# Kernel tuning notes

Hardware: AMD Instinct MI355X
Metric: run time of the kernel (lower is better)

## Reference

```python
import jax, jax.numpy as jnp
import numpy as np

NUM_LAYERS = 2
HIDDEN = 512


def _lstm_layer(x_tbh, h0, c0, Wih, Whh, bih, bhh):
    """Run one LSTM layer over time.
    x_tbh: [T,B,I]; h0,c0: [B,H]; Wih: [4H,I]; Whh: [4H,H]; bih,bhh: [4H].
    Gate order follows torch.nn.LSTMCell: i, f, g, o.
    Returns (outputs [T,B,H], (h_T, c_T)).
    """
    bias = bih + bhh

    def step(carry, x_t):
        h, c = carry
        gates = x_t @ Wih.T + h @ Whh.T + bias  # [B,4H]
        i, f, g, o = jnp.split(gates, 4, axis=-1)
        i = jax.nn.sigmoid(i)
        f = jax.nn.sigmoid(f)
        g = jnp.tanh(g)
        o = jax.nn.sigmoid(o)
        c_new = f * c + i * g
        h_new = o * jnp.tanh(c_new)
        return (h_new, c_new), h_new

    (h_T, c_T), outs = jax.lax.scan(step, (h0, c0), x_tbh)
    return outs, (h_T, c_T)


def setup_inputs() -> dict:
    key = jax.random.key(0)
    ks = jax.random.split(key, 7)
    B, T, I, H, L = 32, 1024, 512, HIDDEN, NUM_LAYERS
    scale = 1.0 / np.sqrt(H)
    return {
        "input": jax.random.normal(ks[0], (B, T, I), dtype=jnp.float32),
        "h0": jax.random.normal(ks[1], (L, B, H), dtype=jnp.float32),
        "c0": jax.random.normal(ks[2], (L, B, H), dtype=jnp.float32),
        "W_ih": jax.random.normal(ks[3], (L, 4 * H, I), dtype=jnp.float32) * scale,
        "W_hh": jax.random.normal(ks[4], (L, 4 * H, H), dtype=jnp.float32) * scale,
        "b_ih": jax.random.normal(ks[5], (L, 4 * H), dtype=jnp.float32) * scale,
        "b_hh": jax.random.normal(ks[6], (L, 4 * H), dtype=jnp.float32) * scale,
    }


def reference(input, h0, c0, W_ih, W_hh, b_ih, b_hh):
    # batch_first=True -> transpose to time-major for the scan
    x = jnp.transpose(input, (1, 0, 2))  # [T,B,I]
    h_outs, c_outs = [], []
    for l in range(NUM_LAYERS):
        x, (h_T, c_T) = _lstm_layer(x, h0[l], c0[l], W_ih[l], W_hh[l], b_ih[l], b_hh[l])
        h_outs.append(h_T)
        c_outs.append(c_T)
    out = jnp.transpose(x, (1, 0, 2))  # back to [B,T,H]
    return out, (jnp.stack(h_outs), jnp.stack(c_outs))
```

## Files before the change

### kernel.cpp

```cpp
#include <hip/hip_runtime.h>
#include <math.h>

#define T_STEPS 1024
#define BATCH   32
#define HID     512
#define G4      2048
#define KDIM    1024
#define NWG     128
#define WGL     64
#define JPW     8
#define APAD    1032
#define FPAD    32

#define OUT_ELEMS   (BATCH * T_STEPS * HID)
#define H_OFF       OUT_ELEMS
#define C_OFF       (OUT_ELEMS + 2 * BATCH * HID)

typedef __attribute__((ext_vector_type(8)))  short short8;
typedef __attribute__((ext_vector_type(16))) float f32x16;

__device__ __forceinline__ unsigned short f2bf(float f) {
    union { float f; unsigned u; } v; v.f = f;
    unsigned r = v.u + 0x7fffu + ((v.u >> 16) & 1u);
    return (unsigned short)(r >> 16);
}

__device__ __forceinline__ float sigm(float x)  { return 1.0f / (1.0f + __expf(-x)); }
__device__ __forceinline__ float ftanh(float x) { return 1.0f - 2.0f / (__expf(2.0f * x) + 1.0f); }

__device__ __forceinline__ short8 load_b128_llc(const void* p) {
    short8 r;
    asm volatile("global_load_dwordx4 %0, %1, off sc0 sc1"
                 : "=v"(r) : "v"(p));
    return r;
}

__device__ __forceinline__ void g_arrive(unsigned* flags, int wg, unsigned epoch, int tid) {
    asm volatile("s_waitcnt vmcnt(0)" ::: "memory");
    __syncthreads();
    if (tid == 0)
        __hip_atomic_store(&flags[wg * FPAD], epoch, __ATOMIC_RELAXED, __HIP_MEMORY_SCOPE_AGENT);
}

__device__ __forceinline__ void g_wait(unsigned* flags, unsigned epoch, int tid) {
    if (tid < NWG) {
        while (__hip_atomic_load(&flags[tid * FPAD], __ATOMIC_RELAXED, __HIP_MEMORY_SCOPE_AGENT) < epoch)
            __builtin_amdgcn_s_sleep(1);
    }
    __syncthreads();
}

__global__ void init_flags(unsigned* flags) {
    for (int i = threadIdx.x; i < NWG * FPAD; i += 256) flags[i] = 0u;
}

__global__ void __launch_bounds__(256, 1)
lstm_persist(const float* __restrict__ x_in,
             const float* __restrict__ h0,
             const float* __restrict__ c0,
             const float* __restrict__ Wih,
             const float* __restrict__ Whh,
             const float* __restrict__ bih,
             const float* __restrict__ bhh,
             float* __restrict__ out,
             unsigned* __restrict__ flags,
             unsigned short* __restrict__ h1ring,
             unsigned short* __restrict__ h2ring,
             unsigned short* __restrict__ xbf,
             int use_xbf)
{
    __shared__ __attribute__((aligned(16))) short Wbuf[32 * APAD];
    __shared__ float gatebuf[4][BATCH][36];
    __shared__ float biasbuf[32];

    const int wg    = blockIdx.x;
    const int layer = (wg >= WGL) ? 1 : 0;
    const int wgl   = wg - layer * WGL;
    const int jbase = wgl * JPW;
    const int tid   = threadIdx.x;

    if (use_xbf) {
        const size_t total4 = (size_t)BATCH * T_STEPS * HID / 4;
        unsigned long long* dst = (unsigned long long*)xbf;
        for (size_t idx = (size_t)wg * 256 + tid; idx < total4; idx += (size_t)NWG * 256) {
            float4 v = *(const float4*)(x_in + idx * 4);
            unsigned long long pk = (unsigned long long)f2bf(v.x)
                                  | ((unsigned long long)f2bf(v.y) << 16)
                                  | ((unsigned long long)f2bf(v.z) << 32)
                                  | ((unsigned long long)f2bf(v.w) << 48);
            dst[idx] = pk;
        }
        __builtin_amdgcn_fence(__ATOMIC_RELEASE, "agent");
    }

    {
        const int lr = tid >> 3;
        const int g0 = tid & 7;
        const int gg = lr >> 3, jloc = lr & 7;
        const int r  = gg * HID + jbase + jloc;
        const float* srcA = Wih + ((size_t)layer * G4 + r) * HID;
        const float* srcB = Whh + ((size_t)layer * G4 + r) * HID;
        short* dstrow = &Wbuf[lr * APAD];
        #pragma unroll
        for (int i = 0; i < 16; ++i) {
            int g = g0 + 8 * i;
            const float* src = (g < 64) ? (srcA + g * 8) : (srcB + (g - 64) * 8);
            float4 v0 = *(const float4*)(src);
            float4 v1 = *(const float4*)(src + 4);
            short8 p;
            p[0] = (short)f2bf(v0.x); p[1] = (short)f2bf(v0.y);
            p[2] = (short)f2bf(v0.z); p[3] = (short)f2bf(v0.w);
            p[4] = (short)f2bf(v1.x); p[5] = (short)f2bf(v1.y);
            p[6] = (short)f2bf(v1.z); p[7] = (short)f2bf(v1.w);
            *(short8*)(dstrow + g * 8) = p;
        }
    }
    if (tid < 32) {
        const int g = tid >> 3, jloc = tid & 7;
        const int r = g * HID + jbase + jloc;
        biasbuf[tid] = bih[(size_t)layer * G4 + r] + bhh[(size_t)layer * G4 + r];
    }

    const int m  = tid >> 3;
    const int jl = tid & 7;
    const int jg = jbase + jl;

    float creg = c0[((size_t)layer * BATCH + m) * HID + jg];

    {
        unsigned hb = (unsigned)f2bf(h0[((size_t)layer * BATCH + m) * HID + jg]);
        unsigned ob = __shfl_xor(hb, 1);
        if ((tid & 1) == 0) {
            unsigned val = hb | (ob << 16);
            unsigned short* ring = (layer == 0) ? h1ring : h2ring;
            if (layer == 0) {
                unsigned* p = (unsigned*)(ring + ((size_t)1 * BATCH + m) * HID + (jg & ~1));
                __hip_atomic_store(p, val, __ATOMIC_RELAXED, __HIP_MEMORY_SCOPE_AGENT);
            } else {
                unsigned* p0 = (unsigned*)(ring + ((size_t)0 * BATCH + m) * HID + (jg & ~1));
                unsigned* p1 = (unsigned*)(ring + ((size_t)1 * BATCH + m) * HID + (jg & ~1));
                __hip_atomic_store(p0, val, __ATOMIC_RELAXED, __HIP_MEMORY_SCOPE_AGENT);
                __hip_atomic_store(p1, val, __ATOMIC_RELAXED, __HIP_MEMORY_SCOPE_AGENT);
            }
        }
    }

    g_arrive(flags, wg, 1u, tid);
    g_wait(flags, 1u, tid);
    __builtin_amdgcn_fence(__ATOMIC_ACQUIRE, "agent");

    const int lane = tid & 63;
    const int wv   = tid >> 6;
    const int hi   = lane >> 5;
    const int arow = lane & 31;
    const int kq   = (wv & 1) * 256;
    const bool xw  = (wv < 2);

    const short* wrow = &Wbuf[arow * APAD + wv * 256 + hi * 8];

    short8 afr[16];

#define PREFETCH_X(tt)                                                        \
    do {                                                                      \
        if (use_xbf) {                                                        \
            const short* bx = (const short*)xbf +                             \
                ((size_t)arow * T_STEPS + (tt)) * HID + kq + hi * 8;          \
            _Pragma("unroll")                                                 \
            for (int j = 0; j < 16; ++j)                                      \
                afr[j] = *(const short8*)(bx + j * 16);                       \
        } else {                                                              \
            const float* fx = x_in +                                          \
                ((size_t)arow * T_STEPS + (tt)) * HID + kq + hi * 8;          \
            _Pragma("unroll")                                                 \
            for (int j = 0; j < 16; ++j) {                                    \
                float4 v0 = *(const float4*)(fx + j * 16);                    \
                float4 v1 = *(const float4*)(fx + j * 16 + 4);                \
                short8 p;                                                     \
                p[0] = (short)f2bf(v0.x); p[1] = (short)f2bf(v0.y);           \
                p[2] = (short)f2bf(v0.z); p[3] = (short)f2bf(v0.w);           \
                p[4] = (short)f2bf(v1.x); p[5] = (short)f2bf(v1.y);           \
                p[6] = (short)f2bf(v1.z); p[7] = (short)f2bf(v1.w);           \
                afr[j] = p;                                                   \
            }                                                                 \
        }                                                                     \
    } while (0)

    if (layer == 0 && xw) PREFETCH_X(0);

    for (int s = 0; s <= T_STEPS; ++s) {
        const int t = (layer == 0) ? s : s - 1;
        const bool active = (t >= 0) && (t < T_STEPS);
        float hv = 0.0f;
        if (active) {
            const int rs = (s + 1) & 1;

            if (!(layer == 0 && xw)) {
                const unsigned short* ring =
                    (layer == 0) ? h1ring : (xw ? h1ring : h2ring);
                const short* base = (const short*)ring +
                    ((size_t)rs * BATCH + arow) * HID + kq + hi * 8;
                #pragma unroll
                for (int j = 0; j < 16; ++j)
                    afr[j] = load_b128_llc(base + j * 16);
                asm volatile("s_waitcnt vmcnt(0)" ::: "memory");
                __builtin_amdgcn_sched_barrier(0);
            }

            f32x16 acc0, acc1;
            #pragma unroll
            for (int r = 0; r < 16; ++r) { acc0[r] = 0.0f; acc1[r] = 0.0f; }
            #pragma unroll
            for (int j = 0; j < 16; j += 2) {
                short8 b0 = *(const short8*)(wrow + j * 16);
                short8 b1 = *(const short8*)(wrow + j * 16 + 16);
                acc0 = __builtin_amdgcn_mfma_f32_32x32x16_bf16(afr[j],     b0, acc0, 0, 0, 0);
                acc1 = __builtin_amdgcn_mfma_f32_32x32x16_bf16(afr[j + 1], b1, acc1, 0, 0, 0);
            }
            #pragma unroll
            for (int r = 0; r < 16; ++r)
                gatebuf[wv][(r & 3) + 8 * (r >> 2) + 4 * hi][arow] = acc0[r] + acc1[r];
            __syncthreads();

            float gi = gatebuf[0][m][jl]      + gatebuf[1][m][jl]
                     + gatebuf[2][m][jl]      + gatebuf[3][m][jl]      + biasbuf[jl];
            float gf = gatebuf[0][m][8 + jl]  + gatebuf[1][m][8 + jl]
                     + gatebuf[2][m][8 + jl]  + gatebuf[3][m][8 + jl]  + biasbuf[8 + jl];
            float gg = gatebuf[0][m][16 + jl] + gatebuf[1][m][16 + jl]
                     + gatebuf[2][m][16 + jl] + gatebuf[3][m][16 + jl] + biasbuf[16 + jl];
            float go = gatebuf[0][m][24 + jl] + gatebuf[1][m][24 + jl]
                     + gatebuf[2][m][24 + jl] + gatebuf[3][m][24 + jl] + biasbuf[24 + jl];
            float iv = sigm(gi), fv = sigm(gf), gv = ftanh(gg), ov = sigm(go);
            creg = fv * creg + iv * gv;
            hv = ov * ftanh(creg);

            {
                const int wslot = s & 1;
                unsigned hb = (unsigned)f2bf(hv);
                unsigned ob = __shfl_xor(hb, 1);
                if ((tid & 1) == 0) {
                    unsigned val = hb | (ob << 16);
                    unsigned short* ringw = (layer == 0) ? h1ring : h2ring;
                    unsigned* p = (unsigned*)(ringw + ((size_t)wslot * BATCH + m) * HID + (jg & ~1));
                    __hip_atomic_store(p, val, __ATOMIC_RELAXED, __HIP_MEMORY_SCOPE_AGENT);
                }
            }
            if (t == T_STEPS - 1)
                out[H_OFF + ((size_t)layer * BATCH + m) * HID + jg] = hv;
        }

        const bool last = (s == T_STEPS);
        if (!last) g_arrive(flags, wg, (unsigned)(s + 2), tid);

        if (active && layer == 1)
            out[((size_t)m * T_STEPS + t) * HID + jg] = hv;
        if (layer == 0 && xw && active && t + 1 < T_STEPS)
            PREFETCH_X(t + 1);

        if (!last) g_wait(flags, (unsigned)(s + 2), tid);
    }

    out[C_OFF + ((size_t)layer * BATCH + m) * HID + jg] = creg;
#undef PREFETCH_X
}

extern "C" void kernel_launch(void* const* d_in, const int* in_sizes, int n_in,
                              void* d_out, int out_size, void* d_ws, size_t ws_size,
                              hipStream_t stream) {
    const float* x   = (const float*)d_in[0];
    const float* h0  = (const float*)d_in[1];
    const float* c0  = (const float*)d_in[2];
    const float* Wih = (const float*)d_in[3];
    const float* Whh = (const float*)d_in[4];
    const float* bih = (const float*)d_in[5];
    const float* bhh = (const float*)d_in[6];
    float* out = (float*)d_out;

    unsigned char* ws = (unsigned char*)d_ws;
    unsigned* flags = (unsigned*)ws;
    unsigned short* h1ring = (unsigned short*)(ws + 16384);
    unsigned short* h2ring = h1ring + 2 * BATCH * HID;
    unsigned short* xbf    = h2ring + 2 * BATCH * HID;

    const size_t xbf_need = 16384 + 2 * 64 * 1024 +
                            (size_t)BATCH * T_STEPS * HID * 2 + 4096;
    int use_xbf = (ws_size >= xbf_need) ? 1 : 0;

    hipLaunchKernelGGL(init_flags, dim3(1), dim3(256), 0, stream, flags);

    void* args[] = { (void*)&x, (void*)&h0, (void*)&c0, (void*)&Wih, (void*)&Whh,
                     (void*)&bih, (void*)&bhh, (void*)&out, (void*)&flags,
                     (void*)&h1ring, (void*)&h2ring, (void*)&xbf, (void*)&use_xbf };
    hipError_t e = hipLaunchCooperativeKernel((void*)lstm_persist, dim3(NWG), dim3(256),
                                              args, 0, stream);
    if (e != hipSuccess) {
        hipLaunchKernelGGL(lstm_persist, dim3(NWG), dim3(256), 0, stream,
                           x, h0, c0, Wih, Whh, bih, bhh, out, flags,
                           h1ring, h2ring, xbf, use_xbf);
    }
}
```

Baseline: 4.652 ms.

## Replace global barrier with per-layer flag waits, 8-slot h1 ring, register-resident weights

Replaces the full all-workgroup barrier each step with targeted flag polling. Layer 1 waits only on layer 0's flags for its input h1 and on its own layer's flags for h2. Layer 0 waits on its own peers, with a lagged check on layer 1 so the 8-slot h1 ring is not overwritten early. Layer 1 now runs two steps behind and prefetches the h1 input fragments before the barrier completes. Weights move from LDS into per-lane bf16 MFMA operand registers, which removes LDS reads from the inner loop at the cost of higher register pressure and more complex correctness invariants.

```diff
diff --git a/kernel.cpp b/kernel.cpp
--- a/kernel.cpp
+++ b/kernel.cpp
@@ -5,16 +5,20 @@
 #define BATCH   32
 #define HID     512
 #define G4      2048
-#define KDIM    1024
 #define NWG     128
 #define WGL     64
 #define JPW     8
-#define APAD    1032
 #define FPAD    32
-
-#define OUT_ELEMS   (BATCH * T_STEPS * HID)
-#define H_OFF       OUT_ELEMS
-#define C_OFF       (OUT_ELEMS + 2 * BATCH * HID)
+#define RD      8
+
+#define WS_FLAGS 0
+#define WS_H1    16384
+#define WS_H2    278528
+#define WS_XBF   344064
+
+#define OUT_ELEMS (BATCH * T_STEPS * HID)
+#define H_OFF OUT_ELEMS
+#define C_OFF (OUT_ELEMS + 2 * BATCH * HID)
 
 typedef __attribute__((ext_vector_type(8)))  short short8;
 typedef __attribute__((ext_vector_type(16))) float f32x16;
@@ -24,14 +28,12 @@
     unsigned r = v.u + 0x7fffu + ((v.u >> 16) & 1u);
     return (unsigned short)(r >> 16);
 }
-
 __device__ __forceinline__ float sigm(float x)  { return 1.0f / (1.0f + __expf(-x)); }
 __device__ __forceinline__ float ftanh(float x) { return 1.0f - 2.0f / (__expf(2.0f * x) + 1.0f); }
 
-__device__ __forceinline__ short8 load_b128_llc(const void* p) {
+__device__ __forceinline__ short8 ld_llc(const void* p) {
     short8 r;
-    asm volatile("global_load_dwordx4 %0, %1, off sc0 sc1"
-                 : "=v"(r) : "v"(p));
+    asm volatile("global_load_dwordx4 %0, %1, off sc0 sc1" : "=v"(r) : "v"(p));
     return r;
 }
 
@@ -42,12 +44,9 @@
         __hip_atomic_store(&flags[wg * FPAD], epoch, __ATOMIC_RELAXED, __HIP_MEMORY_SCOPE_AGENT);
 }
 
-__device__ __forceinline__ void g_wait(unsigned* flags, unsigned epoch, int tid) {
-    if (tid < NWG) {
-        while (__hip_atomic_load(&flags[tid * FPAD], __ATOMIC_RELAXED, __HIP_MEMORY_SCOPE_AGENT) < epoch)
-            __builtin_amdgcn_s_sleep(1);
-    }
-    __syncthreads();
+__device__ __forceinline__ void poll_ge(const unsigned* p, unsigned epoch) {
+    while (__hip_atomic_load(p, __ATOMIC_RELAXED, __HIP_MEMORY_SCOPE_AGENT) < epoch)
+        __builtin_amdgcn_s_sleep(1);
 }
 
 __global__ void init_flags(unsigned* flags) {
@@ -63,13 +62,9 @@
              const float* __restrict__ bih,
              const float* __restrict__ bhh,
              float* __restrict__ out,
-             unsigned* __restrict__ flags,
-             unsigned short* __restrict__ h1ring,
-             unsigned short* __restrict__ h2ring,
-             unsigned short* __restrict__ xbf,
+             unsigned char* __restrict__ ws,
              int use_xbf)
 {
-    __shared__ __attribute__((aligned(16))) short Wbuf[32 * APAD];
     __shared__ float gatebuf[4][BATCH][36];
     __shared__ float biasbuf[32];
 
@@ -78,6 +73,11 @@
     const int wgl   = wg - layer * WGL;
     const int jbase = wgl * JPW;
     const int tid   = threadIdx.x;
+
+    unsigned* flags = (unsigned*)(ws + WS_FLAGS);
+    unsigned short* h1ring = (unsigned short*)(ws + WS_H1);
+    unsigned short* h2ring = (unsigned short*)(ws + WS_H2);
+    unsigned short* xbf    = (unsigned short*)(ws + WS_XBF);
 
     if (use_xbf) {
         const size_t total4 = (size_t)BATCH * T_STEPS * HID / 4;
@@ -93,32 +93,32 @@
         __builtin_amdgcn_fence(__ATOMIC_RELEASE, "agent");
     }
 
-    {
-        const int lr = tid >> 3;
-        const int g0 = tid & 7;
-        const int gg = lr >> 3, jloc = lr & 7;
-        const int r  = gg * HID + jbase + jloc;
-        const float* srcA = Wih + ((size_t)layer * G4 + r) * HID;
-        const float* srcB = Whh + ((size_t)layer * G4 + r) * HID;
-        short* dstrow = &Wbuf[lr * APAD];
-        #pragma unroll
-        for (int i = 0; i < 16; ++i) {
-            int g = g0 + 8 * i;
-            const float* src = (g < 64) ? (srcA + g * 8) : (srcB + (g - 64) * 8);
-            float4 v0 = *(const float4*)(src);
-            float4 v1 = *(const float4*)(src + 4);
-            short8 p;
-            p[0] = (short)f2bf(v0.x); p[1] = (short)f2bf(v0.y);
-            p[2] = (short)f2bf(v0.z); p[3] = (short)f2bf(v0.w);
-            p[4] = (short)f2bf(v1.x); p[5] = (short)f2bf(v1.y);
-            p[6] = (short)f2bf(v1.z); p[7] = (short)f2bf(v1.w);
-            *(short8*)(dstrow + g * 8) = p;
-        }
-    }
     if (tid < 32) {
         const int g = tid >> 3, jloc = tid & 7;
         const int r = g * HID + jbase + jloc;
         biasbuf[tid] = bih[(size_t)layer * G4 + r] + bhh[(size_t)layer * G4 + r];
+    }
+
+    const int lane = tid & 63;
+    const int wv   = tid >> 6;
+    const int hi   = lane >> 5;
+    const int l31  = lane & 31;
+    const int kb   = (wv & 1) * 256;
+
+    short8 bW[16];
+    {
+        const float* Wsel = ((wv < 2) ? Wih : Whh) + (size_t)layer * G4 * HID;
+        const int r = (l31 >> 3) * HID + jbase + (l31 & 7);
+        const float* wr = Wsel + (size_t)r * HID + kb + hi * 8;
+        #pragma unroll
+        for (int j = 0; j < 16; ++j) {
+            float4 v0 = *(const float4*)(wr + j * 16);
+            float4 v1 = *(const float4*)(wr + j * 16 + 4);
+            short8 p;
+            p[0]=(short)f2bf(v0.x); p[1]=(short)f2bf(v0.y); p[2]=(short)f2bf(v0.z); p[3]=(short)f2bf(v0.w);
+            p[4]=(short)f2bf(v1.x); p[5]=(short)f2bf(v1.y); p[6]=(short)f2bf(v1.z); p[7]=(short)f2bf(v1.w);
+            bW[j] = p;
+        }
     }
 
     const int m  = tid >> 3;
@@ -132,13 +132,12 @@
         unsigned ob = __shfl_xor(hb, 1);
         if ((tid & 1) == 0) {
             unsigned val = hb | (ob << 16);
-            unsigned short* ring = (layer == 0) ? h1ring : h2ring;
             if (layer == 0) {
-                unsigned* p = (unsigned*)(ring + ((size_t)1 * BATCH + m) * HID + (jg & ~1));
+                unsigned* p = (unsigned*)(h1ring + ((size_t)7 * BATCH + m) * HID + (jg & ~1));
                 __hip_atomic_store(p, val, __ATOMIC_RELAXED, __HIP_MEMORY_SCOPE_AGENT);
             } else {
-                unsigned* p0 = (unsigned*)(ring + ((size_t)0 * BATCH + m) * HID + (jg & ~1));
-                unsigned* p1 = (unsigned*)(ring + ((size_t)1 * BATCH + m) * HID + (jg & ~1));
+                unsigned* p0 = (unsigned*)(h2ring + ((size_t)0 * BATCH + m) * HID + (jg & ~1));
+                unsigned* p1 = (unsigned*)(h2ring + ((size_t)1 * BATCH + m) * HID + (jg & ~1));
                 __hip_atomic_store(p0, val, __ATOMIC_RELAXED, __HIP_MEMORY_SCOPE_AGENT);
                 __hip_atomic_store(p1, val, __ATOMIC_RELAXED, __HIP_MEMORY_SCOPE_AGENT);
             }
@@ -146,85 +145,79 @@
     }
 
     g_arrive(flags, wg, 1u, tid);
-    g_wait(flags, 1u, tid);
+    if (tid < NWG) poll_ge(flags + tid * FPAD, 1u);
+    __syncthreads();
     __builtin_amdgcn_fence(__ATOMIC_ACQUIRE, "agent");
 
-    const int lane = tid & 63;
-    const int wv   = tid >> 6;
-    const int hi   = lane >> 5;
-    const int arow = lane & 31;
-    const int kq   = (wv & 1) * 256;
-    const bool xw  = (wv < 2);
-
-    const short* wrow = &Wbuf[arow * APAD + wv * 256 + hi * 8];
+    const unsigned* fL0 = flags;
+    const unsigned* fL1 = flags + WGL * FPAD;
 
     short8 afr[16];
 
-#define PREFETCH_X(tt)                                                        \
+#define PREFX(tt)                                                             \
     do {                                                                      \
         if (use_xbf) {                                                        \
             const short* bx = (const short*)xbf +                             \
-                ((size_t)arow * T_STEPS + (tt)) * HID + kq + hi * 8;          \
+                ((size_t)l31 * T_STEPS + (tt)) * HID + kb + hi * 8;           \
             _Pragma("unroll")                                                 \
             for (int j = 0; j < 16; ++j)                                      \
                 afr[j] = *(const short8*)(bx + j * 16);                       \
         } else {                                                              \
             const float* fx = x_in +                                          \
-                ((size_t)arow * T_STEPS + (tt)) * HID + kq + hi * 8;          \
+                ((size_t)l31 * T_STEPS + (tt)) * HID + kb + hi * 8;           \
             _Pragma("unroll")                                                 \
             for (int j = 0; j < 16; ++j) {                                    \
                 float4 v0 = *(const float4*)(fx + j * 16);                    \
                 float4 v1 = *(const float4*)(fx + j * 16 + 4);                \
                 short8 p;                                                     \
-                p[0] = (short)f2bf(v0.x); p[1] = (short)f2bf(v0.y);           \
-                p[2] = (short)f2bf(v0.z); p[3] = (short)f2bf(v0.w);           \
-                p[4] = (short)f2bf(v1.x); p[5] = (short)f2bf(v1.y);           \
-                p[6] = (short)f2bf(v1.z); p[7] = (short)f2bf(v1.w);           \
+                p[0]=(short)f2bf(v0.x); p[1]=(short)f2bf(v0.y);               \
+                p[2]=(short)f2bf(v0.z); p[3]=(short)f2bf(v0.w);               \
+                p[4]=(short)f2bf(v1.x); p[5]=(short)f2bf(v1.y);               \
+                p[6]=(short)f2bf(v1.z); p[7]=(short)f2bf(v1.w);               \
                 afr[j] = p;                                                   \
             }                                                                 \
         }                                                                     \
     } while (0)
 
-    if (layer == 0 && xw) PREFETCH_X(0);
-
-    for (int s = 0; s <= T_STEPS; ++s) {
-        const int t = (layer == 0) ? s : s - 1;
+    if (layer == 0 && wv < 2) PREFX(0);
+
+    const int SE = T_STEPS + 2;
+    for (int s = 0; s <= SE; ++s) {
+        const int t = (layer == 0) ? s : s - 2;
         const bool active = (t >= 0) && (t < T_STEPS);
+        const bool last = (s == SE);
         float hv = 0.0f;
+
         if (active) {
-            const int rs = (s + 1) & 1;
-
-            if (!(layer == 0 && xw)) {
-                const unsigned short* ring =
-                    (layer == 0) ? h1ring : (xw ? h1ring : h2ring);
+            if (wv >= 2) {
+                const unsigned short* ring = (layer == 0) ? h1ring : h2ring;
+                const size_t slot = (layer == 0) ? (size_t)((s - 1) & 7)
+                                                 : (size_t)((s + 1) & 1);
                 const short* base = (const short*)ring +
-                    ((size_t)rs * BATCH + arow) * HID + kq + hi * 8;
+                    (slot * BATCH + l31) * HID + kb + hi * 8;
                 #pragma unroll
-                for (int j = 0; j < 16; ++j)
-                    afr[j] = load_b128_llc(base + j * 16);
-                asm volatile("s_waitcnt vmcnt(0)" ::: "memory");
-                __builtin_amdgcn_sched_barrier(0);
-            }
+                for (int j = 0; j < 16; ++j) afr[j] = ld_llc(base + j * 16);
+            }
+            asm volatile("s_waitcnt vmcnt(0)" ::: "memory");
+            __builtin_amdgcn_sched_barrier(0);
 
             f32x16 acc0, acc1;
             #pragma unroll
-            for (int r = 0; r < 16; ++r) { acc0[r] = 0.0f; acc1[r] = 0.0f; }
+            for (int r = 0; r < 16; ++r) { acc0[r] = 0.f; acc1[r] = 0.f; }
             #pragma unroll
             for (int j = 0; j < 16; j += 2) {
-                short8 b0 = *(const short8*)(wrow + j * 16);
-                short8 b1 = *(const short8*)(wrow + j * 16 + 16);
-                acc0 = __builtin_amdgcn_mfma_f32_32x32x16_bf16(afr[j],     b0, acc0, 0, 0, 0);
-                acc1 = __builtin_amdgcn_mfma_f32_32x32x16_bf16(afr[j + 1], b1, acc1, 0, 0, 0);
+                acc0 = __builtin_amdgcn_mfma_f32_32x32x16_bf16(afr[j],     bW[j],     acc0, 0, 0, 0);
+                acc1 = __builtin_amdgcn_mfma_f32_32x32x16_bf16(afr[j + 1], bW[j + 1], acc1, 0, 0, 0);
             }
             #pragma unroll
             for (int r = 0; r < 16; ++r)
-                gatebuf[wv][(r & 3) + 8 * (r >> 2) + 4 * hi][arow] = acc0[r] + acc1[r];
+                gatebuf[wv][(r & 3) + 8 * (r >> 2) + 4 * hi][l31] = acc0[r] + acc1[r];
             __syncthreads();
 
             float gi = gatebuf[0][m][jl]      + gatebuf[1][m][jl]
                      + gatebuf[2][m][jl]      + gatebuf[3][m][jl]      + biasbuf[jl];
-            float gf = gatebuf[0][m][8 + jl]  + gatebuf[1][m][8 + jl]
-                     + gatebuf[2][m][8 + jl]  + gatebuf[3][m][8 + jl]  + biasbuf[8 + jl];
+            float gf = gatebuf[0][m][8  + jl] + gatebuf[1][m][8  + jl]
+                     + gatebuf[2][m][8  + jl] + gatebuf[3][m][8  + jl] + biasbuf[8  + jl];
             float gg = gatebuf[0][m][16 + jl] + gatebuf[1][m][16 + jl]
                      + gatebuf[2][m][16 + jl] + gatebuf[3][m][16 + jl] + biasbuf[16 + jl];
             float go = gatebuf[0][m][24 + jl] + gatebuf[1][m][24 + jl]
@@ -234,13 +227,15 @@
             hv = ov * ftanh(creg);
 
             {
-                const int wslot = s & 1;
                 unsigned hb = (unsigned)f2bf(hv);
                 unsigned ob = __shfl_xor(hb, 1);
                 if ((tid & 1) == 0) {
                     unsigned val = hb | (ob << 16);
-                    unsigned short* ringw = (layer == 0) ? h1ring : h2ring;
-                    unsigned* p = (unsigned*)(ringw + ((size_t)wslot * BATCH + m) * HID + (jg & ~1));
+                    unsigned* p;
+                    if (layer == 0)
+                        p = (unsigned*)(h1ring + ((size_t)(s & 7) * BATCH + m) * HID + (jg & ~1));
+                    else
+                        p = (unsigned*)(h2ring + ((size_t)(s & 1) * BATCH + m) * HID + (jg & ~1));
                     __hip_atomic_store(p, val, __ATOMIC_RELAXED, __HIP_MEMORY_SCOPE_AGENT);
                 }
             }
@@ -248,19 +243,34 @@
                 out[H_OFF + ((size_t)layer * BATCH + m) * HID + jg] = hv;
         }
 
-        const bool last = (s == T_STEPS);
-        if (!last) g_arrive(flags, wg, (unsigned)(s + 2), tid);
-
-        if (active && layer == 1)
-            out[((size_t)m * T_STEPS + t) * HID + jg] = hv;
-        if (layer == 0 && xw && active && t + 1 < T_STEPS)
-            PREFETCH_X(t + 1);
-
-        if (!last) g_wait(flags, (unsigned)(s + 2), tid);
+        if (!last) {
+            g_arrive(flags, wg, (unsigned)(s + 2), tid);
+
+            if (layer == 1) {
+                if (active)
+                    out[((size_t)m * T_STEPS + t) * HID + jg] = hv;
+                if (wv < 2 && s >= 1 && s <= T_STEPS) {
+                    poll_ge(fL0 + lane * FPAD, (unsigned)(s + 1));
+                    const short* base = (const short*)h1ring +
+                        ((size_t)((s - 1) & 7) * BATCH + l31) * HID + kb + hi * 8;
+                    #pragma unroll
+                    for (int j = 0; j < 16; ++j) afr[j] = ld_llc(base + j * 16);
+                }
+                if (wv == 3)
+                    poll_ge(fL1 + lane * FPAD, (unsigned)(s + 2));
+            } else {
+                if (wv < 2 && active && t + 1 < T_STEPS) PREFX(t + 1);
+                if (wv == 2 && s >= 7)
+                    poll_ge(fL1 + lane * FPAD, (unsigned)(s - 3));
+                if (wv == 3)
+                    poll_ge(fL0 + lane * FPAD, (unsigned)(s + 2));
+            }
+            __syncthreads();
+        }
     }
 
     out[C_OFF + ((size_t)layer * BATCH + m) * HID + jg] = creg;
-#undef PREFETCH_X
+#undef PREFX
 }
 
 extern "C" void kernel_launch(void* const* d_in, const int* in_sizes, int n_in,
@@ -274,27 +284,19 @@
     const float* bih = (const float*)d_in[5];
     const float* bhh = (const float*)d_in[6];
     float* out = (float*)d_out;
-
     unsigned char* ws = (unsigned char*)d_ws;
-    unsigned* flags = (unsigned*)ws;
-    unsigned short* h1ring = (unsigned short*)(ws + 16384);
-    unsigned short* h2ring = h1ring + 2 * BATCH * HID;
-    unsigned short* xbf    = h2ring + 2 * BATCH * HID;
-
-    const size_t xbf_need = 16384 + 2 * 64 * 1024 +
-                            (size_t)BATCH * T_STEPS * HID * 2 + 4096;
+
+    const size_t xbf_need = (size_t)WS_XBF + (size_t)BATCH * T_STEPS * HID * 2;
     int use_xbf = (ws_size >= xbf_need) ? 1 : 0;
 
-    hipLaunchKernelGGL(init_flags, dim3(1), dim3(256), 0, stream, flags);
+    hipLaunchKernelGGL(init_flags, dim3(1), dim3(256), 0, stream, (unsigned*)ws);
 
     void* args[] = { (void*)&x, (void*)&h0, (void*)&c0, (void*)&Wih, (void*)&Whh,
-                     (void*)&bih, (void*)&bhh, (void*)&out, (void*)&flags,
-                     (void*)&h1ring, (void*)&h2ring, (void*)&xbf, (void*)&use_xbf };
+                     (void*)&bih, (void*)&bhh, (void*)&out, (void*)&ws, (void*)&use_xbf };
     hipError_t e = hipLaunchCooperativeKernel((void*)lstm_persist, dim3(NWG), dim3(256),
                                               args, 0, stream);
     if (e != hipSuccess) {
         hipLaunchKernelGGL(lstm_persist, dim3(NWG), dim3(256), 0, stream,
-                           x, h0, c0, Wih, Whh, bih, bhh, out, flags,
-                           h1ring, h2ring, xbf, use_xbf);
-    }
-}
+                           x, h0, c0, Wih, Whh, bih, bhh, out, ws, use_xbf);
+    }
+}
```

New measurement: 4.267 ms. -8.3%, faster.
